# Performance work log

Measured on AMD Instinct MI355X. Metric: run time of the kernel, lower is better.

Reference implementation:

```python
import jax, jax.numpy as jnp
import numpy as np

DIM = 768; NH = 12; HD = 64; H = 32; W = 32; B = 4; HID = 3072
THETA = 10000.0; EPS = 1e-5


def _rope_freqs():
    # _compute_rope_frequencies(head_dim, end_x=W, end_y=H)
    freqs = 1.0 / THETA ** (np.arange(0, HD, 4)[: HD // 4].astype(np.float32) / HD)
    t = np.arange(H * W, dtype=np.float32)
    tx = t % W
    ty = np.floor(t / W)
    f = np.concatenate([np.outer(tx, freqs), np.outer(ty, freqs)], axis=-1)  # (L, HD//2)
    return jnp.asarray(np.cos(f)), jnp.asarray(np.sin(f))


def _layernorm(x, w, b):
    mu = jnp.mean(x, axis=-1, keepdims=True)
    var = jnp.mean(jnp.square(x - mu), axis=-1, keepdims=True)
    return (x - mu) * jax.lax.rsqrt(var + EPS) * w + b


def _rotate(x, cos, sin):
    # x: (B, NH, L, HD); interleaved (even, odd) pair rotation
    xr = x.reshape(x.shape[:-1] + (-1, 2))
    x0, x1 = xr[..., 0], xr[..., 1]
    o0 = x0 * cos - x1 * sin
    o1 = x0 * sin + x1 * cos
    return jnp.stack([o0, o1], axis=-1).reshape(x.shape)


def _forward(x, ln1_w, ln1_b, w_qkv, b_qkv, w_proj, b_proj, rel_pos_h, rel_pos_w,
             ln2_w, ln2_b, w_fc1, b_fc1, w_fc2, b_fc2):
    cos, sin = _rope_freqs()
    shortcut = x
    xn = _layernorm(x, ln1_w, ln1_b)
    L = H * W
    xf = xn.reshape(B, L, DIM)
    qkv = (xf @ w_qkv.T + b_qkv).reshape(B, L, 3, NH, HD).transpose(2, 0, 3, 1, 4)
    q, k, v = qkv[0], qkv[1], qkv[2]  # each (B, NH, L, HD)
    q = _rotate(q, cos, sin)
    k = _rotate(k, cos, sin)
    attn = jnp.einsum('bnqd,bnkd->bnqk', q, k) * (HD ** -0.5)
    # relative position bias (q_size == k_size, so no interpolation/scaling)
    idx_h = np.arange(H)[:, None] - np.arange(H)[None, :] + (H - 1)
    idx_w = np.arange(W)[:, None] - np.arange(W)[None, :] + (W - 1)
    bias_h = rel_pos_h[idx_h]  # (H, H, HD)
    bias_w = rel_pos_w[idx_w]  # (W, W, HD)
    q5 = q.reshape(B, NH, H, W, HD)
    rel_h = jnp.einsum('bnhwc,hkc->bnhwk', q5, bias_h)
    rel_w = jnp.einsum('bnhwc,wkc->bnhwk', q5, bias_w)
    attn = attn.reshape(B, NH, H, W, H, W) + rel_h[..., :, None] + rel_w[..., None, :]
    attn = jax.nn.softmax(attn.reshape(B, NH, L, L), axis=-1)
    out = jnp.einsum('bnqk,bnkd->bnqd', attn, v)
    out = out.transpose(0, 2, 1, 3).reshape(B, H, W, DIM)
    out = out @ w_proj.T + b_proj
    x = shortcut + out
    h = _layernorm(x, ln2_w, ln2_b)
    h = jax.nn.gelu(h @ w_fc1.T + b_fc1, approximate=False)
    return x + (h @ w_fc2.T + b_fc2)


def setup_inputs() -> dict:
    key = jax.random.key(0)
    ks = jax.random.split(key, 8)
    s = 0.02
    return {
        'x': jax.random.normal(ks[0], (B, H, W, DIM), jnp.float32),
        'ln1_w': jnp.ones((DIM,), jnp.float32),
        'ln1_b': jnp.zeros((DIM,), jnp.float32),
        'w_qkv': jax.random.normal(ks[1], (3 * DIM, DIM), jnp.float32) * s,
        'b_qkv': jnp.zeros((3 * DIM,), jnp.float32),
        'w_proj': jax.random.normal(ks[2], (DIM, DIM), jnp.float32) * s,
        'b_proj': jnp.zeros((DIM,), jnp.float32),
        'rel_pos_h': jax.random.normal(ks[3], (2 * H - 1, HD), jnp.float32) * s,
        'rel_pos_w': jax.random.normal(ks[4], (2 * W - 1, HD), jnp.float32) * s,
        'ln2_w': jnp.ones((DIM,), jnp.float32),
        'ln2_b': jnp.zeros((DIM,), jnp.float32),
        'w_fc1': jax.random.normal(ks[5], (HID, DIM), jnp.float32) * s,
        'b_fc1': jnp.zeros((HID,), jnp.float32),
        'w_fc2': jax.random.normal(ks[6], (DIM, HID), jnp.float32) * s,
        'b_fc2': jnp.zeros((DIM,), jnp.float32),
    }


def reference(x, ln1_w, ln1_b, w_qkv, b_qkv, w_proj, b_proj, rel_pos_h, rel_pos_w,
              ln2_w, ln2_b, w_fc1, b_fc1, w_fc2, b_fc2):
    return _forward(x, ln1_w, ln1_b, w_qkv, b_qkv, w_proj, b_proj, rel_pos_h, rel_pos_w,
                    ln2_w, ln2_b, w_fc1, b_fc1, w_fc2, b_fc2)
```

## Files before the change

kernel.cpp:

```cpp
#include <hip/hip_runtime.h>
#include <hip/hip_bf16.h>

#define DIM 768
#define NH 12
#define BB 4
#define LL 1024
#define MM 4096
#define HID 3072

typedef short short8 __attribute__((ext_vector_type(8)));
typedef float f32x4 __attribute__((ext_vector_type(4)));

static __device__ __forceinline__ unsigned short f2bu(float f) {
    unsigned u = __float_as_uint(f);
    u += 0x7fffu + ((u >> 16) & 1u);
    return (unsigned short)(u >> 16);
}
static __device__ __forceinline__ float bu2f(unsigned short u) {
    return __uint_as_float((unsigned)u << 16);
}

__global__ __launch_bounds__(256) void ln_kernel(const float* __restrict__ in,
                                                 const float* __restrict__ g,
                                                 const float* __restrict__ bta,
                                                 unsigned short* __restrict__ out) {
    __shared__ float red[8];
    int row = blockIdx.x;
    int tid = threadIdx.x;
    float v[3];
    float s = 0.f, s2 = 0.f;
#pragma unroll
    for (int i = 0; i < 3; ++i) {
        int c = tid + i*256;
        float x = in[(size_t)row*DIM + c];
        v[i] = x; s += x; s2 += x*x;
    }
#pragma unroll
    for (int off = 32; off; off >>= 1) { s += __shfl_down(s, off); s2 += __shfl_down(s2, off); }
    int wv = tid >> 6;
    if ((tid & 63) == 0) { red[wv] = s; red[4+wv] = s2; }
    __syncthreads();
    if (tid == 0) {
        float a = red[0]+red[1]+red[2]+red[3];
        float b = red[4]+red[5]+red[6]+red[7];
        red[0] = a * (1.f/DIM);
        red[4] = b * (1.f/DIM);
    }
    __syncthreads();
    float mu = red[0];
    float var = red[4] - mu*mu;
    float inv = rsqrtf(var + 1e-5f);
#pragma unroll
    for (int i = 0; i < 3; ++i) {
        int c = tid + i*256;
        out[(size_t)row*DIM + c] = f2bu((v[i]-mu)*inv*g[c] + bta[c]);
    }
}

template<int EPI>
__global__ __launch_bounds__(256) void gemm_mfma(const unsigned short* __restrict__ A,
                                                 const float* __restrict__ W,
                                                 const float* __restrict__ bias,
                                                 const float* __restrict__ res,
                                                 void* __restrict__ out,
                                                 int N, int K) {
    __shared__ unsigned short As[128][40];
    __shared__ unsigned short Bs[128][40];
    int tid = threadIdx.x;
    int m0 = blockIdx.y * 128, n0 = blockIdx.x * 128;
    int wave = tid >> 6, lane = tid & 63;
    int wr = wave >> 1, wc = wave & 1;
    int lr = lane & 15, kg = lane >> 4;
    f32x4 acc[4][4] = {};
    int ar = tid >> 2, ac = (tid & 3) * 8;

    for (int kt = 0; kt < K; kt += 32) {
        __syncthreads();
        *(int4*)&As[ar][ac]    = *(const int4*)&A[(size_t)(m0+ar)*K + kt + ac];
        *(int4*)&As[ar+64][ac] = *(const int4*)&A[(size_t)(m0+ar+64)*K + kt + ac];
#pragma unroll
        for (int h = 0; h < 2; ++h) {
            int r = ar + h*64;
            const float* wp = &W[(size_t)(n0+r)*K + kt + ac];
            float4 w0 = *(const float4*)wp;
            float4 w1 = *(const float4*)(wp + 4);
            short8 wb;
            wb[0]=f2bu(w0.x); wb[1]=f2bu(w0.y); wb[2]=f2bu(w0.z); wb[3]=f2bu(w0.w);
            wb[4]=f2bu(w1.x); wb[5]=f2bu(w1.y); wb[6]=f2bu(w1.z); wb[7]=f2bu(w1.w);
            *(short8*)&Bs[r][ac] = wb;
        }
        __syncthreads();
        short8 af[4], bg[4];
#pragma unroll
        for (int m = 0; m < 4; ++m) af[m] = *(const short8*)&As[wr*64 + m*16 + lr][kg*8];
#pragma unroll
        for (int n = 0; n < 4; ++n) bg[n] = *(const short8*)&Bs[wc*64 + n*16 + lr][kg*8];
#pragma unroll
        for (int m = 0; m < 4; ++m)
#pragma unroll
            for (int n = 0; n < 4; ++n)
                acc[m][n] = __builtin_amdgcn_mfma_f32_16x16x32_bf16(af[m], bg[n], acc[m][n], 0, 0, 0);
    }

#pragma unroll
    for (int m = 0; m < 4; ++m) {
#pragma unroll
        for (int n = 0; n < 4; ++n) {
            int col = n0 + wc*64 + n*16 + lr;
            float bcol = bias[col];
#pragma unroll
            for (int j = 0; j < 4; ++j) {
                int row = m0 + wr*64 + m*16 + kg*4 + j;
                float v = acc[m][n][j] + bcol;
                if (EPI == 3) v += res[(size_t)row*N + col];
                if (EPI == 2) {
                    v = 0.5f*v*(1.f + erff(v*0.70710678118654752f));
                    ((unsigned short*)out)[(size_t)row*N + col] = f2bu(v);
                } else {
                    ((float*)out)[(size_t)row*N + col] = v;
                }
            }
        }
    }
}

__global__ __launch_bounds__(256) void qkv_cvt(const float* __restrict__ qkv,
                                               unsigned short* __restrict__ qb,
                                               unsigned short* __restrict__ kb,
                                               unsigned short* __restrict__ vb) {
    int idx = blockIdx.x*256 + threadIdx.x;
    int t  = idx / 1152;
    int cp = idx - t*1152;
    int col = cp*2;
    int s = col / 768;
    int wi = col - s*768;
    int n = wi >> 6, d = wi & 63;
    float2 v2 = *(const float2*)&qkv[(size_t)t*2304 + col];
    int l = t & (LL-1);
    if (s < 2) {
        int j = d >> 1;
        int pos = (j < 16) ? (l & 31) : (l >> 5);
        float freq = expf(-(float)(j & 15) * 0.0625f * 9.210340371976184f);
        float ang = (float)pos * freq;
        float sn, cs;
        sincosf(ang, &sn, &cs);
        float x0 = v2.x, x1 = v2.y;
        v2.x = x0*cs - x1*sn;
        v2.y = x0*sn + x1*cs;
    }
    unsigned short* dst = (s == 0) ? qb : (s == 1) ? kb : vb;
    int b = t >> 10;
    unsigned pk = (unsigned)f2bu(v2.x) | ((unsigned)f2bu(v2.y) << 16);
    *(unsigned*)&dst[((size_t)(b*NH + n)*LL + l)*64 + d] = pk;
}

__global__ __launch_bounds__(256) void attn_mfma(const unsigned short* __restrict__ qb,
                                                 const unsigned short* __restrict__ kb,
                                                 const unsigned short* __restrict__ vb,
                                                 const float* __restrict__ relh,
                                                 const float* __restrict__ relw,
                                                 unsigned short* __restrict__ out) {
    __shared__ unsigned short Kb[64][72];
    __shared__ unsigned short Vt[64][72];
    __shared__ unsigned short Pb[4][16][72];
    __shared__ float rbh[64][36];
    __shared__ float rbw[64][36];
    __shared__ float sl[128];
    int qt = blockIdx.x, n = blockIdx.y, b = blockIdx.z;
    int tid = threadIdx.x;
    int w = tid >> 6, lane = tid & 63;
    int lr = lane & 15, kg = lane >> 4;
    size_t hb = ((size_t)b*NH + n) * (LL*64);

    {
        int q = tid >> 2, g = tid & 3;
        int qrow = qt*64 + q;
        int qh = qrow >> 5, qw = qrow & 31;
        const unsigned short* qr = qb + hb + (size_t)qrow*64;
        float ah[8] = {}, aw[8] = {};
        for (int d = 0; d < 64; ++d) {
            float qd = bu2f(qr[d]);
#pragma unroll
            for (int i = 0; i < 8; ++i) {
                ah[i] += qd * relh[(size_t)(qh - (g*8+i) + 31)*64 + d];
                aw[i] += qd * relw[(size_t)(qw - (g*8+i) + 31)*64 + d];
            }
        }
#pragma unroll
        for (int i = 0; i < 8; ++i) { rbh[q][g*8+i] = ah[i]; rbw[q][g*8+i] = aw[i]; }
    }

    const unsigned short* qfr = qb + hb + (size_t)(qt*64 + w*16 + lr)*64;
    short8 qf0 = *(const short8*)(qfr + kg*8);
    short8 qf1 = *(const short8*)(qfr + 32 + kg*8);

    f32x4 o[4] = {};
    float mR = -1e30f, lR = 0.f;

    __syncthreads();

    for (int kt = 0; kt < 16; ++kt) {
        __syncthreads();
        {
            int r = tid >> 3, c8 = (tid & 7) * 8;
            const unsigned short* kptr = kb + hb + (size_t)(kt*64)*64;
            *(short8*)&Kb[r][c8]    = *(const short8*)(kptr + (size_t)r*64 + c8);
            *(short8*)&Kb[r+32][c8] = *(const short8*)(kptr + (size_t)(r+32)*64 + c8);
            const unsigned short* vptr = vb + hb + (size_t)(kt*64)*64;
            short8 v0 = *(const short8*)(vptr + (size_t)r*64 + c8);
            short8 v1 = *(const short8*)(vptr + (size_t)(r+32)*64 + c8);
#pragma unroll
            for (int i = 0; i < 8; ++i) { Vt[c8+i][r] = v0[i]; Vt[c8+i][r+32] = v1[i]; }
        }
        __syncthreads();

        f32x4 st[4] = {};
#pragma unroll
        for (int ks = 0; ks < 4; ++ks) {
            short8 kf0 = *(const short8*)&Kb[ks*16 + lr][kg*8];
            short8 kf1 = *(const short8*)&Kb[ks*16 + lr][32 + kg*8];
            st[ks] = __builtin_amdgcn_mfma_f32_16x16x32_bf16(kf0, qf0, st[ks], 0, 0, 0);
            st[ks] = __builtin_amdgcn_mfma_f32_16x16x32_bf16(kf1, qf1, st[ks], 0, 0, 0);
        }
        int q = w*16 + lr;
        float rh0 = rbh[q][kt*2], rh1 = rbh[q][kt*2+1];
        f32x4 rw0 = *(const f32x4*)&rbw[q][kg*4];
        f32x4 rw1 = *(const f32x4*)&rbw[q][16 + kg*4];
        float tmax = -1e30f;
#pragma unroll
        for (int ks = 0; ks < 4; ++ks) {
            float rh = (ks < 2) ? rh0 : rh1;
#pragma unroll
            for (int j = 0; j < 4; ++j) {
                float sv = st[ks][j]*0.125f + rh + ((ks & 1) ? rw1[j] : rw0[j]);
                st[ks][j] = sv;
                tmax = fmaxf(tmax, sv);
            }
        }
        tmax = fmaxf(tmax, __shfl_xor(tmax, 16));
        tmax = fmaxf(tmax, __shfl_xor(tmax, 32));
        float mnew = fmaxf(mR, tmax);
        float sc = __expf(mR - mnew);
        float tsum = 0.f;
        unsigned pw0[4], pw1[4];
#pragma unroll
        for (int ks = 0; ks < 4; ++ks) {
            float e0 = __expf(st[ks][0]-mnew), e1 = __expf(st[ks][1]-mnew);
            float e2 = __expf(st[ks][2]-mnew), e3 = __expf(st[ks][3]-mnew);
            tsum += (e0+e1)+(e2+e3);
            pw0[ks] = (unsigned)f2bu(e0) | ((unsigned)f2bu(e1) << 16);
            pw1[ks] = (unsigned)f2bu(e2) | ((unsigned)f2bu(e3) << 16);
        }
        tsum += __shfl_xor(tsum, 16);
        tsum += __shfl_xor(tsum, 32);
        lR = lR*sc + tsum;
        mR = mnew;
        if (lane < 16) sl[w*16 + lr] = sc;
#pragma unroll
        for (int ks = 0; ks < 4; ++ks)
            *(uint2*)&Pb[w][lr][ks*16 + kg*4] = make_uint2(pw0[ks], pw1[ks]);
        f32x4 sc4 = *(const f32x4*)&sl[w*16 + kg*4];
#pragma unroll
        for (int ds = 0; ds < 4; ++ds) o[ds] *= sc4;
        short8 pf0 = *(const short8*)&Pb[w][lr][kg*8];
        short8 pf1 = *(const short8*)&Pb[w][lr][32 + kg*8];
#pragma unroll
        for (int ds = 0; ds < 4; ++ds) {
            short8 vt0 = *(const short8*)&Vt[ds*16 + lr][kg*8];
            short8 vt1 = *(const short8*)&Vt[ds*16 + lr][32 + kg*8];
            o[ds] = __builtin_amdgcn_mfma_f32_16x16x32_bf16(pf0, vt0, o[ds], 0, 0, 0);
            o[ds] = __builtin_amdgcn_mfma_f32_16x16x32_bf16(pf1, vt1, o[ds], 0, 0, 0);
        }
    }

    if (lane < 16) sl[64 + w*16 + lr] = 1.f / lR;
    f32x4 il4 = *(const f32x4*)&sl[64 + w*16 + kg*4];
#pragma unroll
    for (int ds = 0; ds < 4; ++ds)
#pragma unroll
        for (int j = 0; j < 4; ++j) {
            size_t row = (size_t)b*LL + qt*64 + w*16 + kg*4 + j;
            out[row*DIM + n*64 + ds*16 + lr] = f2bu(o[ds][j] * il4[j]);
        }
}

extern "C" void kernel_launch(void* const* d_in, const int* in_sizes, int n_in,
                              void* d_out, int out_size, void* d_ws, size_t ws_size,
                              hipStream_t stream) {
    const float* x      = (const float*)d_in[0];
    const float* ln1w   = (const float*)d_in[1];
    const float* ln1b   = (const float*)d_in[2];
    const float* w_qkv  = (const float*)d_in[3];
    const float* b_qkv  = (const float*)d_in[4];
    const float* w_proj = (const float*)d_in[5];
    const float* b_proj = (const float*)d_in[6];
    const float* relh   = (const float*)d_in[7];
    const float* relw   = (const float*)d_in[8];
    const float* ln2w   = (const float*)d_in[9];
    const float* ln2b   = (const float*)d_in[10];
    const float* w_fc1  = (const float*)d_in[11];
    const float* b_fc1  = (const float*)d_in[12];
    const float* w_fc2  = (const float*)d_in[13];
    const float* b_fc2  = (const float*)d_in[14];

    char* ws = (char*)d_ws;
    unsigned short* xn   = (unsigned short*)(ws);
    float*          qkv  = (float*)(ws + 6291456);
    unsigned short* aout = (unsigned short*)(ws + 44040192);
    float*          x2   = (float*)(ws + 50331648);
    unsigned short* fc1h = (unsigned short*)(ws + 6291456);
    unsigned short* qb   = (unsigned short*)(ws);
    unsigned short* kb   = (unsigned short*)(ws + 50331648);
    unsigned short* vb   = (unsigned short*)(ws + 56623104);

    ln_kernel<<<MM, 256, 0, stream>>>(x, ln1w, ln1b, xn);
    gemm_mfma<0><<<dim3(18, 32), 256, 0, stream>>>(xn, w_qkv, b_qkv, nullptr, qkv, 2304, 768);
    qkv_cvt<<<18432, 256, 0, stream>>>(qkv, qb, kb, vb);
    attn_mfma<<<dim3(16, NH, BB), 256, 0, stream>>>(qb, kb, vb, relh, relw, aout);
    gemm_mfma<3><<<dim3(6, 32), 256, 0, stream>>>(aout, w_proj, b_proj, x, x2, 768, 768);
    ln_kernel<<<MM, 256, 0, stream>>>(x2, ln2w, ln2b, xn);
    gemm_mfma<2><<<dim3(24, 32), 256, 0, stream>>>(xn, w_fc1, b_fc1, nullptr, fc1h, HID, 768);
    gemm_mfma<3><<<dim3(6, 32), 256, 0, stream>>>(fc1h, w_fc2, b_fc2, x2, (float*)d_out, 768, 3072);
}
```

Baseline: 531.4 us.

## Prefetch K/V tiles into registers, remap blocks for XCD locality, vectorize rel-pos bias

The attention kernel now loads the next K/V tile from global memory into registers while the current tile is computed, then commits it to shared memory after the PV MFMAs, hiding global load latency. V is transposed by strided global gathers so the LDS writes become vectorized short8 stores instead of scattered scalar stores. The block index is remapped so consecutive blocks scheduled on the same XCD share heads, aiming for better L2 reuse of K/V. The relative-position bias dot products use vectorized q and rel_pos loads. The cost is more registers and uncoalesced scalar 2-byte global reads for V.

```diff
diff --git a/kernel.cpp b/kernel.cpp
--- a/kernel.cpp
+++ b/kernel.cpp
@@ -166,11 +166,41 @@
     __shared__ float rbh[64][36];
     __shared__ float rbw[64][36];
     __shared__ float sl[128];
-    int qt = blockIdx.x, n = blockIdx.y, b = blockIdx.z;
+
+    int p = blockIdx.x + 16*(blockIdx.y + 12*blockIdx.z);
+    int wg = (p & 7)*96 + (p >> 3);
+    int qt = wg & 15, n = (wg >> 4) % 12, b = (wg >> 4) / 12;
+
     int tid = threadIdx.x;
     int w = tid >> 6, lane = tid & 63;
     int lr = lane & 15, kg = lane >> 4;
     size_t hb = ((size_t)b*NH + n) * (LL*64);
+
+    const unsigned short* kbase = kb + hb;
+    const unsigned short* vbase = vb + hb;
+
+    int sr = tid >> 3, sc8 = (tid & 7) * 8;
+    int vd = tid & 63, vco = tid >> 6;
+
+    short8 kpre0, kpre1, vpre0, vpre1;
+    auto load_tile = [&](int kt) {
+        const unsigned short* kp = kbase + (size_t)(kt*64)*64;
+        kpre0 = *(const short8*)(kp + (size_t)sr*64 + sc8);
+        kpre1 = *(const short8*)(kp + (size_t)(sr+32)*64 + sc8);
+        const unsigned short* vp = vbase + (size_t)(kt*64)*64;
+#pragma unroll
+        for (int i = 0; i < 8; ++i) vpre0[i] = (short)vp[(size_t)(vco*8 + i)*64 + vd];
+#pragma unroll
+        for (int i = 0; i < 8; ++i) vpre1[i] = (short)vp[(size_t)((vco+4)*8 + i)*64 + vd];
+    };
+    auto commit_tile = [&]() {
+        *(short8*)&Kb[sr][sc8]        = kpre0;
+        *(short8*)&Kb[sr+32][sc8]     = kpre1;
+        *(short8*)&Vt[vd][vco*8]      = vpre0;
+        *(short8*)&Vt[vd][vco*8 + 32] = vpre1;
+    };
+
+    load_tile(0);
 
     {
         int q = tid >> 2, g = tid & 3;
@@ -178,12 +208,22 @@
         int qh = qrow >> 5, qw = qrow & 31;
         const unsigned short* qr = qb + hb + (size_t)qrow*64;
         float ah[8] = {}, aw[8] = {};
-        for (int d = 0; d < 64; ++d) {
-            float qd = bu2f(qr[d]);
+#pragma unroll
+        for (int d8 = 0; d8 < 8; ++d8) {
+            short8 qv = *(const short8*)(qr + d8*8);
+            float qf[8];
+#pragma unroll
+            for (int i2 = 0; i2 < 8; ++i2) qf[i2] = bu2f((unsigned short)qv[i2]);
 #pragma unroll
             for (int i = 0; i < 8; ++i) {
-                ah[i] += qd * relh[(size_t)(qh - (g*8+i) + 31)*64 + d];
-                aw[i] += qd * relw[(size_t)(qw - (g*8+i) + 31)*64 + d];
+                const float* rh = &relh[(size_t)(qh - (g*8+i) + 31)*64 + d8*8];
+                const float* rw = &relw[(size_t)(qw - (g*8+i) + 31)*64 + d8*8];
+                float4 h0 = *(const float4*)rh, h1 = *(const float4*)(rh+4);
+                float4 w0 = *(const float4*)rw, w1 = *(const float4*)(rw+4);
+                ah[i] += qf[0]*h0.x + qf[1]*h0.y + qf[2]*h0.z + qf[3]*h0.w
+                       + qf[4]*h1.x + qf[5]*h1.y + qf[6]*h1.z + qf[7]*h1.w;
+                aw[i] += qf[0]*w0.x + qf[1]*w0.y + qf[2]*w0.z + qf[3]*w0.w
+                       + qf[4]*w1.x + qf[5]*w1.y + qf[6]*w1.z + qf[7]*w1.w;
             }
         }
 #pragma unroll
@@ -197,22 +237,11 @@
     f32x4 o[4] = {};
     float mR = -1e30f, lR = 0.f;
 
+    commit_tile();
     __syncthreads();
 
     for (int kt = 0; kt < 16; ++kt) {
-        __syncthreads();
-        {
-            int r = tid >> 3, c8 = (tid & 7) * 8;
-            const unsigned short* kptr = kb + hb + (size_t)(kt*64)*64;
-            *(short8*)&Kb[r][c8]    = *(const short8*)(kptr + (size_t)r*64 + c8);
-            *(short8*)&Kb[r+32][c8] = *(const short8*)(kptr + (size_t)(r+32)*64 + c8);
-            const unsigned short* vptr = vb + hb + (size_t)(kt*64)*64;
-            short8 v0 = *(const short8*)(vptr + (size_t)r*64 + c8);
-            short8 v1 = *(const short8*)(vptr + (size_t)(r+32)*64 + c8);
-#pragma unroll
-            for (int i = 0; i < 8; ++i) { Vt[c8+i][r] = v0[i]; Vt[c8+i][r+32] = v1[i]; }
-        }
-        __syncthreads();
+        if (kt < 15) load_tile(kt+1);
 
         f32x4 st[4] = {};
 #pragma unroll
@@ -270,6 +299,12 @@
             short8 vt1 = *(const short8*)&Vt[ds*16 + lr][32 + kg*8];
             o[ds] = __builtin_amdgcn_mfma_f32_16x16x32_bf16(pf0, vt0, o[ds], 0, 0, 0);
             o[ds] = __builtin_amdgcn_mfma_f32_16x16x32_bf16(pf1, vt1, o[ds], 0, 0, 0);
+        }
+
+        if (kt < 15) {
+            __syncthreads();
+            commit_tile();
+            __syncthreads();
         }
     }
 
```

Result: faster. 443.3 us (-16.6%).
